# Performance work log

Measured on AMD Instinct MI355X. Metric: run time of the kernel, lower is better.

Reference implementation:

```python
import jax, jax.numpy as jnp
import numpy as np

S, L, E, H, HID, T = 4096, 16, 256, 512, 512, 50
CHAR_V = 128


def _lstm_scan(x, W_ih, W_hh, b):
    """x: [T, B, D] -> all hidden states [T, B, H]. PyTorch gate order i,f,g,o.
    b is the sum of torch's b_ih + b_hh (identical math)."""
    Hh = W_hh.shape[1]
    B = x.shape[1]

    def cell(carry, xt):
        h, c = carry
        g = xt @ W_ih.T + h @ W_hh.T + b  # [B, 4H]
        i, f, gg, o = jnp.split(g, 4, axis=-1)
        c = jax.nn.sigmoid(f) * c + jax.nn.sigmoid(i) * jnp.tanh(gg)
        h = jax.nn.sigmoid(o) * jnp.tanh(c)
        return (h, c), h

    init = (jnp.zeros((B, Hh), x.dtype), jnp.zeros((B, Hh), x.dtype))
    _, hs = jax.lax.scan(cell, init, x)
    return hs


def setup_inputs() -> dict:
    key = jax.random.key(0)
    ks = jax.random.split(key, 18)

    def p(k, shape):
        return jax.random.normal(k, shape, jnp.float32) * 0.05

    return {
        "chars": jax.random.randint(ks[0], (S, L), 0, CHAR_V),
        "char_lens": jax.random.randint(ks[1], (S,), 0, L),
        "char_table": p(ks[2], (CHAR_V, E)),
        "cW_ih": p(ks[3], (4 * E, E)),
        "cW_hh": p(ks[4], (4 * E, E)),
        "cb": p(ks[5], (4 * E,)),
        "W_ih0": p(ks[6], (2, 4 * H, E)),
        "W_hh0": p(ks[7], (2, 4 * H, H)),
        "b0": p(ks[8], (2, 4 * H)),
        "W_ih1": p(ks[9], (2, 4 * H, 2 * H)),
        "W_hh1": p(ks[10], (2, 4 * H, H)),
        "b1": p(ks[11], (2, 4 * H)),
        "fc1_w": p(ks[12], (HID, 2 * H)),
        "fc1_b": p(ks[13], (HID,)),
        "fc2_w": p(ks[14], (T, HID)),
        "fc2_b": p(ks[15], (T,)),
    }


def reference(chars, char_lens, char_table, cW_ih, cW_hh, cb,
              W_ih0, W_hh0, b0, W_ih1, W_hh1, b1,
              fc1_w, fc1_b, fc2_w, fc2_b):
    n_words = chars.shape[0]
    # --- char LSTM: batched over all words (replaces per-word python loop) ---
    emb = char_table[chars]                               # [S, L, E]
    hs = _lstm_scan(emb.transpose(1, 0, 2), cW_ih, cW_hh, cb)  # [L, S, E]
    lens = jnp.maximum(char_lens, 1)                      # every word has >=1 char
    word_emb = hs[lens - 1, jnp.arange(n_words)]          # hn per word: [S, E]

    # --- 2-layer bidirectional sentence LSTM, batch = 1 ---
    x = word_emb[:, None, :]                              # [S, 1, E]

    def bi_layer(x, Wih, Whh, b):
        fwd = _lstm_scan(x, Wih[0], Whh[0], b[0])
        bwd = _lstm_scan(x[::-1], Wih[1], Whh[1], b[1])[::-1]
        return jnp.concatenate([fwd, bwd], axis=-1)       # [S, 1, 2H]

    x = bi_layer(x, W_ih0, W_hh0, b0)
    x = bi_layer(x, W_ih1, W_hh1, b1)

    # --- MLP head ---
    out = x[:, 0, :]                                      # [S, 2H]
    out = jnp.tanh(out @ fc1_w.T + fc1_b)                 # [S, HID]
    return out @ fc2_w.T + fc2_b                          # [S, T]
```

## Files before the change

kernel.cpp:

```cpp
#include <hip/hip_runtime.h>
#include <math.h>
#include <stdint.h>


#define NPOS 4096
#define GDIM 2048

__device__ __forceinline__ float sigf(float x) { return 1.0f / (1.0f + __expf(-x)); }
__device__ __forceinline__ float tanh_fast(float x) {
  float e = __expf(2.f * x);
  return 1.f - 2.f / (e + 1.f);
}

__global__ __launch_bounds__(256) void build_wt_kernel(
    const float* __restrict__ cWih, const float* __restrict__ cWhh,
    float* __restrict__ Wt)
{
  __shared__ float tile[64][65];
  const int k0 = blockIdx.x * 64;
  const int g0 = blockIdx.y * 64;
  const float* src = (k0 < 256) ? cWih : cWhh;
  const int sk0 = k0 & 255;
  for (int i = threadIdx.x; i < 64 * 64; i += 256) {
    int r = i >> 6, cc = i & 63;
    tile[r][cc] = src[(size_t)(g0 + r) * 256 + sk0 + cc];
  }
  __syncthreads();
  for (int i = threadIdx.x; i < 64 * 64; i += 256) {
    int kk = i >> 6, gg = i & 63;
    Wt[(size_t)(k0 + kk) * 1024 + g0 + gg] = tile[gg][kk];
  }
}

__global__ __launch_bounds__(256) void char_lstm_kernel(
    const int* __restrict__ chars, const int* __restrict__ lens,
    const float* __restrict__ table, const float* __restrict__ Wt,
    const float* __restrict__ cb, float* __restrict__ word_emb)
{
  __shared__ float u[8][512];
  __shared__ float wt[8][1024];
  __shared__ int sidx[8];
  const int tid = threadIdx.x;
  const int ch = tid;
  const int w0 = blockIdx.x * 8;
  if (tid < 8) { int l = lens[w0 + tid]; sidx[tid] = (l < 1 ? 1 : l) - 1; }
  float c[8], acc0[8], acc1[8], acc2[8], acc3[8];
  #pragma unroll
  for (int w = 0; w < 8; ++w) { u[w][256 + ch] = 0.f; c[w] = 0.f; }
  const float cb0 = cb[ch], cb1 = cb[256 + ch], cb2 = cb[512 + ch], cb3 = cb[768 + ch];

  for (int t = 0; t < 16; ++t) {
    for (int w = 0; w < 8; ++w) {
      int cid = chars[(w0 + w) * 16 + t];
      u[w][ch] = table[(size_t)cid * 256 + ch];
    }
    #pragma unroll
    for (int w = 0; w < 8; ++w) { acc0[w] = cb0; acc1[w] = cb1; acc2[w] = cb2; acc3[w] = cb3; }
    for (int k0 = 0; k0 < 512; k0 += 8) {
      #pragma unroll
      for (int r = 0; r < 8; ++r)
        ((float4*)&wt[r][0])[tid] = ((const float4*)(Wt + (size_t)(k0 + r) * 1024))[tid];
      __syncthreads();
      #pragma unroll
      for (int kk = 0; kk < 8; ++kk) {
        const float wv0 = wt[kk][ch], wv1 = wt[kk][256 + ch];
        const float wv2 = wt[kk][512 + ch], wv3 = wt[kk][768 + ch];
        #pragma unroll
        for (int w = 0; w < 8; ++w) {
          const float uv = u[w][k0 + kk];
          acc0[w] = fmaf(wv0, uv, acc0[w]);
          acc1[w] = fmaf(wv1, uv, acc1[w]);
          acc2[w] = fmaf(wv2, uv, acc2[w]);
          acc3[w] = fmaf(wv3, uv, acc3[w]);
        }
      }
      __syncthreads();
    }
    #pragma unroll
    for (int w = 0; w < 8; ++w) {
      float iv = sigf(acc0[w]), fv = sigf(acc1[w]);
      float gv = tanhf(acc2[w]), ov = sigf(acc3[w]);
      c[w] = fv * c[w] + iv * gv;
      float h = ov * tanhf(c[w]);
      u[w][256 + ch] = h;
      if (t == sidx[w]) word_emb[(size_t)(w0 + w) * 256 + ch] = h;
    }
  }
}

#define SW(c) ((c) + (((c) >> 3) << 2))
template <int SPLIT, int ACT, int PERM>
__global__ __launch_bounds__(256) void gemm_kernel(
    const float* __restrict__ A, const float* __restrict__ A2,
    const float* __restrict__ B, const float* __restrict__ bias,
    float* __restrict__ C, int M, int N, int K)
{
  __shared__ float At[8 * 192];
  __shared__ float Bt[8 * 192];
  const int tid = threadIdx.x;
  const int bm0 = blockIdx.x * 128, bn0 = blockIdx.y * 128;
  float acc[8][8];
  #pragma unroll
  for (int i = 0; i < 8; ++i)
    #pragma unroll
    for (int j = 0; j < 8; ++j) acc[i][j] = 0.f;
  const int sr = tid >> 1;
  const int sk = (tid & 1) * 4;
  const int tm = (tid >> 4) * 8, tn = (tid & 15) * 8;
  const int swsr = SW(sr);
  const int stm = SW(tm), stn = SW(tn);
  for (int k0 = 0; k0 < K; k0 += 8) {
    const int kg = k0 + sk;
    float4 av;
    if (SPLIT) {
      const float* srcp = (kg < 512) ? A : A2;
      av = *(const float4*)(srcp + (size_t)(bm0 + sr) * 512 + (kg & 511));
    } else {
      av = *(const float4*)(A + (size_t)(bm0 + sr) * K + kg);
    }
    float4 bv = {0.f, 0.f, 0.f, 0.f};
    if (bn0 + sr < N) bv = *(const float4*)(B + (size_t)(bn0 + sr) * K + kg);
    At[(sk + 0) * 192 + swsr] = av.x; At[(sk + 1) * 192 + swsr] = av.y;
    At[(sk + 2) * 192 + swsr] = av.z; At[(sk + 3) * 192 + swsr] = av.w;
    Bt[(sk + 0) * 192 + swsr] = bv.x; Bt[(sk + 1) * 192 + swsr] = bv.y;
    Bt[(sk + 2) * 192 + swsr] = bv.z; Bt[(sk + 3) * 192 + swsr] = bv.w;
    __syncthreads();
    #pragma unroll
    for (int kk = 0; kk < 8; ++kk) {
      float a[8], b[8];
      *(float4*)&a[0] = *(const float4*)&At[kk * 192 + stm];
      *(float4*)&a[4] = *(const float4*)&At[kk * 192 + stm + 4];
      *(float4*)&b[0] = *(const float4*)&Bt[kk * 192 + stn];
      *(float4*)&b[4] = *(const float4*)&Bt[kk * 192 + stn + 4];
      #pragma unroll
      for (int i = 0; i < 8; ++i)
        #pragma unroll
        for (int j = 0; j < 8; ++j) acc[i][j] = fmaf(a[i], b[j], acc[i][j]);
    }
    __syncthreads();
  }
  #pragma unroll
  for (int i = 0; i < 8; ++i) {
    const int m = bm0 + tm + i;
    float* crow = C + (size_t)m * N;
    #pragma unroll
    for (int j = 0; j < 8; ++j) {
      const int n = bn0 + tn + j;
      if (n < N) {
        float v = acc[i][j] + bias[n];
        if (ACT) v = tanhf(v);
        if (PERM) crow[((n & 511) << 2) | (n >> 9)] = v;
        else      crow[n] = v;
      }
    }
  }
}

__global__ __launch_bounds__(512) void scan_kernel(
    const float* __restrict__ Xf, const float* __restrict__ Xb,
    const float* __restrict__ Whf, const float* __restrict__ Whb,
    unsigned long long* __restrict__ Tf, unsigned long long* __restrict__ Tb,
    float* __restrict__ Hf, float* __restrict__ Hb)
{
  __shared__ float lds_h[2][576];
  const int tid = threadIdx.x;
  const int dir = blockIdx.x & 1;
  const int wg  = blockIdx.x >> 1;
  const float* X = dir ? Xb : Xf;
  const float* Wh = dir ? Whb : Whf;
  unsigned long long* T = dir ? Tb : Tf;
  float* Hd = dir ? Hb : Hf;

  const int row8 = tid >> 3;
  const int klane = tid & 7;
  const int u = row8 >> 2, g = row8 & 3;
  const int R = g * 512 + wg * 16 + u;

  float wreg[64];
  {
    const float* wrow = Wh + (size_t)R * 512 + klane * 64;
    #pragma unroll
    for (int i = 0; i < 16; ++i) {
      float4 v = ((const float4*)wrow)[i];
      wreg[4 * i] = v.x; wreg[4 * i + 1] = v.y; wreg[4 * i + 2] = v.z; wreg[4 * i + 3] = v.w;
    }
  }
  const int l0 = 72 * klane;
  const int l1 = l0 + 36;
  const int la = tid + ((tid >> 5) << 2);
  const int rep = wg & 3;

  for (int i = tid; i < 576; i += 512) lds_h[0][i] = 0.f;

  const bool xl = (klane == 0);
  const int xoff = wg * 64 + row8;
  float xcur = 0.f, xnxt = 0.f;
  if (xl) {
    xcur = X[(size_t)(dir ? NPOS - 1 : 0) * GDIM + xoff];
    xnxt = X[(size_t)(dir ? NPOS - 2 : 1) * GDIM + xoff];
  }
  float creg = 0.f;
  __syncthreads();

  for (int s = 0; s < NPOS; ++s) {
    const int p = dir ? (NPOS - 1 - s) : s;
    if (s > 0) {
      const unsigned int tg = (unsigned int)s;
      const unsigned long long* w =
          T + (size_t)((rep << 1) | ((s - 1) & 1)) * 512 + tid;
      unsigned long long v;
      do { v = __hip_atomic_load(w, __ATOMIC_RELAXED, __HIP_MEMORY_SCOPE_AGENT); }
      while ((unsigned int)(v >> 32) != tg);
      lds_h[s & 1][la] = __uint_as_float((unsigned int)v);
    }
    __syncthreads();
    const float* hb = &lds_h[s & 1][0];
    float sA = xl ? xcur : 0.f, sB = 0.f, sC = 0.f, sD = 0.f;
    if (xl) {
      xcur = xnxt;
      if (s + 2 < NPOS) xnxt = X[(size_t)(dir ? NPOS - 3 - s : s + 2) * GDIM + xoff];
    }
    #pragma unroll
    for (int i = 0; i < 4; ++i) {
      float4 a = *(const float4*)&hb[l0 + 4 * i];
      sA = fmaf(wreg[4 * i + 0], a.x, sA);
      sA = fmaf(wreg[4 * i + 1], a.y, sA);
      sA = fmaf(wreg[4 * i + 2], a.z, sA);
      sA = fmaf(wreg[4 * i + 3], a.w, sA);
      float4 b = *(const float4*)&hb[l0 + 16 + 4 * i];
      sB = fmaf(wreg[16 + 4 * i + 0], b.x, sB);
      sB = fmaf(wreg[16 + 4 * i + 1], b.y, sB);
      sB = fmaf(wreg[16 + 4 * i + 2], b.z, sB);
      sB = fmaf(wreg[16 + 4 * i + 3], b.w, sB);
      float4 c = *(const float4*)&hb[l1 + 4 * i];
      sC = fmaf(wreg[32 + 4 * i + 0], c.x, sC);
      sC = fmaf(wreg[32 + 4 * i + 1], c.y, sC);
      sC = fmaf(wreg[32 + 4 * i + 2], c.z, sC);
      sC = fmaf(wreg[32 + 4 * i + 3], c.w, sC);
      float4 d = *(const float4*)&hb[l1 + 16 + 4 * i];
      sD = fmaf(wreg[48 + 4 * i + 0], d.x, sD);
      sD = fmaf(wreg[48 + 4 * i + 1], d.y, sD);
      sD = fmaf(wreg[48 + 4 * i + 2], d.z, sD);
      sD = fmaf(wreg[48 + 4 * i + 3], d.w, sD);
    }
    float sum = (sA + sB) + (sC + sD);
    sum += __shfl_xor(sum, 1);
    sum += __shfl_xor(sum, 2);
    sum += __shfl_xor(sum, 4);
    const int base = (tid & 63) & ~31;
    float gf = __shfl(sum, base + 8);
    float gg = __shfl(sum, base + 16);
    float go = __shfl(sum, base + 24);
    if ((tid & 31) == 0) {
      float iv = sigf(sum), fv = sigf(gf), gv = tanh_fast(gg), ov = sigf(go);
      creg = fv * creg + iv * gv;
      float h = ov * tanh_fast(creg);
      const int j = wg * 16 + u;
      unsigned long long pack = ((unsigned long long)(unsigned int)(s + 1) << 32)
                              | (unsigned long long)__float_as_uint(h);
      #pragma unroll
      for (int r2 = 0; r2 < 4; ++r2)
        __hip_atomic_store(&T[(size_t)((r2 << 1) | (s & 1)) * 512 + j], pack,
                           __ATOMIC_RELAXED, __HIP_MEMORY_SCOPE_AGENT);
      Hd[(size_t)p * 512 + j] = h;
    }
  }
}

extern "C" void kernel_launch(void* const* d_in, const int* in_sizes, int n_in,
                              void* d_out, int out_size, void* d_ws, size_t ws_size,
                              hipStream_t stream) {
  const int* chars = (const int*)d_in[0];
  const int* lens = (const int*)d_in[1];
  const float* table = (const float*)d_in[2];
  const float* cWih = (const float*)d_in[3];
  const float* cWhh = (const float*)d_in[4];
  const float* cb = (const float*)d_in[5];
  const float* Wih0 = (const float*)d_in[6];
  const float* Whh0 = (const float*)d_in[7];
  const float* b0 = (const float*)d_in[8];
  const float* Wih1 = (const float*)d_in[9];
  const float* Whh1 = (const float*)d_in[10];
  const float* b1 = (const float*)d_in[11];
  const float* fc1w = (const float*)d_in[12];
  const float* fc1b = (const float*)d_in[13];
  const float* fc2w = (const float*)d_in[14];
  const float* fc2b = (const float*)d_in[15];
  float* out = (float*)d_out;

  char* ws = (char*)d_ws;
  size_t off = 0;
  auto alloc = [&](size_t bytes) -> void* {
    void* p = ws + off;
    off += (bytes + 255) & ~(size_t)255;
    return p;
  };
  float* word_emb = (float*)alloc((size_t)4096 * 256 * 4);
  float* X0f = (float*)alloc((size_t)4096 * 2048 * 4);
  float* X0b = (float*)alloc((size_t)4096 * 2048 * 4);
  float* H0f = (float*)alloc((size_t)4096 * 512 * 4);
  float* H0b = (float*)alloc((size_t)4096 * 512 * 4);
  float* H1f = (float*)alloc((size_t)4096 * 512 * 4);
  float* H1b = (float*)alloc((size_t)4096 * 512 * 4);
  float* fc1out = (float*)alloc((size_t)4096 * 512 * 4);
  float* Wt = (float*)alloc((size_t)512 * 1024 * 4);
  unsigned long long* Tall = (unsigned long long*)alloc((size_t)4 * 4096 * 8);
  unsigned long long* T0f = Tall;
  unsigned long long* T0b = Tall + 4096;
  unsigned long long* T1f = Tall + 8192;
  unsigned long long* T1b = Tall + 12288;
  if (off > ws_size) return;

  hipMemsetAsync(Tall, 0, (size_t)4 * 4096 * 8, stream);

  build_wt_kernel<<<dim3(8, 16), 256, 0, stream>>>(cWih, cWhh, Wt);
  char_lstm_kernel<<<512, 256, 0, stream>>>(chars, lens, table, Wt, cb, word_emb);

  gemm_kernel<0, 0, 1><<<dim3(32, 16), 256, 0, stream>>>(
      word_emb, nullptr, Wih0, b0, X0f, 4096, 2048, 256);
  gemm_kernel<0, 0, 1><<<dim3(32, 16), 256, 0, stream>>>(
      word_emb, nullptr, Wih0 + (size_t)2048 * 256, b0 + 2048, X0b, 4096, 2048, 256);
  scan_kernel<<<64, 512, 0, stream>>>(X0f, X0b, Whh0, Whh0 + (size_t)2048 * 512,
                                      T0f, T0b, H0f, H0b);

  gemm_kernel<1, 0, 1><<<dim3(32, 16), 256, 0, stream>>>(
      H0f, H0b, Wih1, b1, X0f, 4096, 2048, 1024);
  gemm_kernel<1, 0, 1><<<dim3(32, 16), 256, 0, stream>>>(
      H0f, H0b, Wih1 + (size_t)2048 * 1024, b1 + 2048, X0b, 4096, 2048, 1024);
  scan_kernel<<<64, 512, 0, stream>>>(X0f, X0b, Whh1, Whh1 + (size_t)2048 * 512,
                                      T1f, T1b, H1f, H1b);

  gemm_kernel<1, 1, 0><<<dim3(32, 4), 256, 0, stream>>>(
      H1f, H1b, fc1w, fc1b, fc1out, 4096, 512, 1024);
  gemm_kernel<0, 0, 0><<<dim3(32, 1), 256, 0, stream>>>(
      fc1out, nullptr, fc2w, fc2b, out, 4096, 50, 512);
}
```

Before: 16.06 ms.

## Co-locate each scan direction on one XCD and use per-step L2-local flags

The scan grid is enlarged so that, with blockIdx & 7 selecting a slot, only slots 0 and 1 do work; this appears intended to place all forward blocks on one XCD and all backward blocks on another, so they can exchange hidden states through that XCD's shared L2 instead of device-scope atomics. The exchange buffer becomes one slot per timestep, tagged with the position, which removes the 4-way replicated stores and the double-buffer reuse. Polling uses inline-asm loads with sc0 and falls back to agent-scope atomic loads after 512 spins. In exchange, the flag buffer grows to 64 MB and must be memset every call, and correctness relies on the block-to-XCD placement and cache bits behaving as assumed.

```diff
diff --git a/kernel.cpp b/kernel.cpp
--- a/kernel.cpp
+++ b/kernel.cpp
@@ -162,10 +162,12 @@
     unsigned long long* __restrict__ Tf, unsigned long long* __restrict__ Tb,
     float* __restrict__ Hf, float* __restrict__ Hb)
 {
+  const int slot = blockIdx.x & 7;
+  if (slot >= 2) return;
+  const int dir = slot;
+  const int wg  = blockIdx.x >> 3;
   __shared__ float lds_h[2][576];
   const int tid = threadIdx.x;
-  const int dir = blockIdx.x & 1;
-  const int wg  = blockIdx.x >> 1;
   const float* X = dir ? Xb : Xf;
   const float* Wh = dir ? Whb : Whf;
   unsigned long long* T = dir ? Tb : Tf;
@@ -188,7 +190,6 @@
   const int l0 = 72 * klane;
   const int l1 = l0 + 36;
   const int la = tid + ((tid >> 5) << 2);
-  const int rep = wg & 3;
 
   for (int i = tid; i < 576; i += 512) lds_h[0][i] = 0.f;
 
@@ -200,17 +201,29 @@
     xnxt = X[(size_t)(dir ? NPOS - 2 : 1) * GDIM + xoff];
   }
   float creg = 0.f;
+  bool loc_ok = true;
   __syncthreads();
 
   for (int s = 0; s < NPOS; ++s) {
     const int p = dir ? (NPOS - 1 - s) : s;
     if (s > 0) {
-      const unsigned int tg = (unsigned int)s;
-      const unsigned long long* w =
-          T + (size_t)((rep << 1) | ((s - 1) & 1)) * 512 + tid;
+      const int pprev = dir ? (NPOS - s) : (s - 1);
+      const unsigned int tg = (unsigned int)(pprev + 1);
+      const unsigned long long* wp = T + (size_t)pprev * 512 + tid;
       unsigned long long v;
-      do { v = __hip_atomic_load(w, __ATOMIC_RELAXED, __HIP_MEMORY_SCOPE_AGENT); }
-      while ((unsigned int)(v >> 32) != tg);
+      if (loc_ok) {
+        int spins = 0;
+        for (;;) {
+          asm volatile("global_load_dwordx2 %0, %1, off sc0\n\ts_waitcnt vmcnt(0)"
+                       : "=v"(v) : "v"(wp) : "memory");
+          if ((unsigned int)(v >> 32) == tg) break;
+          if (++spins > 512) { loc_ok = false; break; }
+        }
+      }
+      if (!loc_ok) {
+        do { v = __hip_atomic_load(wp, __ATOMIC_RELAXED, __HIP_MEMORY_SCOPE_AGENT); }
+        while ((unsigned int)(v >> 32) != tg);
+      }
       lds_h[s & 1][la] = __uint_as_float((unsigned int)v);
     }
     __syncthreads();
@@ -256,12 +269,11 @@
       creg = fv * creg + iv * gv;
       float h = ov * tanh_fast(creg);
       const int j = wg * 16 + u;
-      unsigned long long pack = ((unsigned long long)(unsigned int)(s + 1) << 32)
+      unsigned long long pack = ((unsigned long long)(unsigned int)(p + 1) << 32)
                               | (unsigned long long)__float_as_uint(h);
-      #pragma unroll
-      for (int r2 = 0; r2 < 4; ++r2)
-        __hip_atomic_store(&T[(size_t)((r2 << 1) | (s & 1)) * 512 + j], pack,
-                           __ATOMIC_RELAXED, __HIP_MEMORY_SCOPE_AGENT);
+      unsigned long long* sp = T + (size_t)p * 512 + j;
+      asm volatile("global_store_dwordx2 %0, %1, off sc0" :: "v"(sp), "v"(pack) : "memory");
+      asm volatile("global_store_dwordx2 %0, %1, off sc0 sc1" :: "v"(sp), "v"(pack) : "memory");
       Hd[(size_t)p * 512 + j] = h;
     }
   }
@@ -304,14 +316,14 @@
   float* H1b = (float*)alloc((size_t)4096 * 512 * 4);
   float* fc1out = (float*)alloc((size_t)4096 * 512 * 4);
   float* Wt = (float*)alloc((size_t)512 * 1024 * 4);
-  unsigned long long* Tall = (unsigned long long*)alloc((size_t)4 * 4096 * 8);
+  unsigned long long* Tall = (unsigned long long*)alloc((size_t)4 * 4096 * 512 * 8);
   unsigned long long* T0f = Tall;
-  unsigned long long* T0b = Tall + 4096;
-  unsigned long long* T1f = Tall + 8192;
-  unsigned long long* T1b = Tall + 12288;
+  unsigned long long* T0b = Tall + (size_t)4096 * 512;
+  unsigned long long* T1f = Tall + (size_t)2 * 4096 * 512;
+  unsigned long long* T1b = Tall + (size_t)3 * 4096 * 512;
   if (off > ws_size) return;
 
-  hipMemsetAsync(Tall, 0, (size_t)4 * 4096 * 8, stream);
+  hipMemsetAsync(Tall, 0, (size_t)4 * 4096 * 512 * 8, stream);
 
   build_wt_kernel<<<dim3(8, 16), 256, 0, stream>>>(cWih, cWhh, Wt);
   char_lstm_kernel<<<512, 256, 0, stream>>>(chars, lens, table, Wt, cb, word_emb);
@@ -320,15 +332,15 @@
       word_emb, nullptr, Wih0, b0, X0f, 4096, 2048, 256);
   gemm_kernel<0, 0, 1><<<dim3(32, 16), 256, 0, stream>>>(
       word_emb, nullptr, Wih0 + (size_t)2048 * 256, b0 + 2048, X0b, 4096, 2048, 256);
-  scan_kernel<<<64, 512, 0, stream>>>(X0f, X0b, Whh0, Whh0 + (size_t)2048 * 512,
-                                      T0f, T0b, H0f, H0b);
+  scan_kernel<<<256, 512, 0, stream>>>(X0f, X0b, Whh0, Whh0 + (size_t)2048 * 512,
+                                       T0f, T0b, H0f, H0b);
 
   gemm_kernel<1, 0, 1><<<dim3(32, 16), 256, 0, stream>>>(
       H0f, H0b, Wih1, b1, X0f, 4096, 2048, 1024);
   gemm_kernel<1, 0, 1><<<dim3(32, 16), 256, 0, stream>>>(
       H0f, H0b, Wih1 + (size_t)2048 * 1024, b1 + 2048, X0b, 4096, 2048, 1024);
-  scan_kernel<<<64, 512, 0, stream>>>(X0f, X0b, Whh1, Whh1 + (size_t)2048 * 512,
-                                      T1f, T1b, H1f, H1b);
+  scan_kernel<<<256, 512, 0, stream>>>(X0f, X0b, Whh1, Whh1 + (size_t)2048 * 512,
+                                       T1f, T1b, H1f, H1b);
 
   gemm_kernel<1, 1, 0><<<dim3(32, 4), 256, 0, stream>>>(
       H1f, H1b, fc1w, fc1b, fc1out, 4096, 512, 1024);
```

After: 36.99 ms. 2.3x slower.

## Replace FP32 SIMT input-projection GEMMs with bf16 MFMA GEMM kernel

Applied to the files above, without the earlier changes.

Adds a new GEMM kernel that converts fp32 A and B tiles to bf16 in LDS and computes 128x128 output tiles with 16x16x32 bf16 MFMA instructions. It replaces the scalar-FMA GEMM for the four LSTM input projections and the fc1 layer. The aim is to cut the non-recurrent GEMM time by using matrix cores. In exchange, inputs are rounded to bf16, which lowers precision, and the kernel has no double buffering, so global-load latency is not overlapped.

```diff
diff --git a/kernel.cpp b/kernel.cpp
--- a/kernel.cpp
+++ b/kernel.cpp
@@ -5,11 +5,20 @@
 
 #define NPOS 4096
 #define GDIM 2048
+
+typedef short short8 __attribute__((ext_vector_type(8)));
+typedef float f32x4 __attribute__((ext_vector_type(4)));
 
 __device__ __forceinline__ float sigf(float x) { return 1.0f / (1.0f + __expf(-x)); }
 __device__ __forceinline__ float tanh_fast(float x) {
   float e = __expf(2.f * x);
   return 1.f - 2.f / (e + 1.f);
+}
+__device__ __forceinline__ unsigned int pack_bf16(float a, float b) {
+  unsigned int ua = __float_as_uint(a), ub = __float_as_uint(b);
+  ua = (ua + 0x7fffu + ((ua >> 16) & 1u)) >> 16;
+  ub = (ub + 0x7fffu + ((ub >> 16) & 1u)) >> 16;
+  return ua | (ub << 16);
 }
 
 __global__ __launch_bounds__(256) void build_wt_kernel(
@@ -151,6 +160,99 @@
         if (ACT) v = tanhf(v);
         if (PERM) crow[((n & 511) << 2) | (n >> 9)] = v;
         else      crow[n] = v;
+      }
+    }
+  }
+}
+
+template <int SPLIT, int ACT, int PERM>
+__global__ __launch_bounds__(256) void mfgemm_kernel(
+    const float* __restrict__ A, const float* __restrict__ A2,
+    const float* __restrict__ B, const float* __restrict__ bias,
+    float* __restrict__ C, int M, int N, int K)
+{
+  __shared__ unsigned short AL[128 * 40];
+  __shared__ unsigned short BL[128 * 40];
+  const int tid = threadIdx.x;
+  const int bm0 = blockIdx.x * 128, bn0 = blockIdx.y * 128;
+  const int srow = tid >> 1;
+  const int sk = (tid & 1) * 16;
+  const int lane = tid & 63;
+  const int wid = tid >> 6;
+  const int wm0 = (wid >> 1) * 64;
+  const int wn0 = (wid & 1) * 64;
+  const int lrow = lane & 15;
+  const int lk = (lane >> 4) * 8;
+
+  f32x4 acc[4][4];
+  #pragma unroll
+  for (int i = 0; i < 4; ++i)
+    #pragma unroll
+    for (int j = 0; j < 4; ++j) acc[i][j] = (f32x4){0.f, 0.f, 0.f, 0.f};
+
+  for (int k0 = 0; k0 < K; k0 += 32) {
+    const int kg = k0 + sk;
+    float av[16], bv[16];
+    if (SPLIT) {
+      const float* srcp = (kg < 512) ? A : A2;
+      const float* ap = srcp + (size_t)(bm0 + srow) * 512 + (kg & 511);
+      #pragma unroll
+      for (int i = 0; i < 4; ++i) *(float4*)&av[4 * i] = ((const float4*)ap)[i];
+      const float* srcq = (kg < 512) ? B : (B + 512);
+      (void)srcq;
+    } else {
+      const float* ap = A + (size_t)(bm0 + srow) * K + kg;
+      #pragma unroll
+      for (int i = 0; i < 4; ++i) *(float4*)&av[4 * i] = ((const float4*)ap)[i];
+    }
+    {
+      const float* bp = B + (size_t)(bn0 + srow) * K + kg;
+      #pragma unroll
+      for (int i = 0; i < 4; ++i) *(float4*)&bv[4 * i] = ((const float4*)bp)[i];
+    }
+    unsigned int pa[8], pb[8];
+    #pragma unroll
+    for (int i = 0; i < 8; ++i) {
+      pa[i] = pack_bf16(av[2 * i], av[2 * i + 1]);
+      pb[i] = pack_bf16(bv[2 * i], bv[2 * i + 1]);
+    }
+    unsigned short* adst = &AL[srow * 40 + sk];
+    unsigned short* bdst = &BL[srow * 40 + sk];
+    *(uint4*)adst       = *(uint4*)&pa[0];
+    *(uint4*)(adst + 8) = *(uint4*)&pa[4];
+    *(uint4*)bdst       = *(uint4*)&pb[0];
+    *(uint4*)(bdst + 8) = *(uint4*)&pb[4];
+    __syncthreads();
+
+    short8 af[4], bf[4];
+    #pragma unroll
+    for (int mi = 0; mi < 4; ++mi)
+      af[mi] = *(const short8*)&AL[(wm0 + mi * 16 + lrow) * 40 + lk];
+    #pragma unroll
+    for (int ni = 0; ni < 4; ++ni)
+      bf[ni] = *(const short8*)&BL[(wn0 + ni * 16 + lrow) * 40 + lk];
+    #pragma unroll
+    for (int mi = 0; mi < 4; ++mi)
+      #pragma unroll
+      for (int ni = 0; ni < 4; ++ni)
+        acc[mi][ni] = __builtin_amdgcn_mfma_f32_16x16x32_bf16(
+            af[mi], bf[ni], acc[mi][ni], 0, 0, 0);
+    __syncthreads();
+  }
+
+  #pragma unroll
+  for (int mi = 0; mi < 4; ++mi) {
+    #pragma unroll
+    for (int ni = 0; ni < 4; ++ni) {
+      const int n = bn0 + wn0 + ni * 16 + (lane & 15);
+      const float bz = bias[n];
+      const int nw = PERM ? (((n & 511) << 2) | (n >> 9)) : n;
+      #pragma unroll
+      for (int r = 0; r < 4; ++r) {
+        const int m = bm0 + wm0 + mi * 16 + (lane >> 4) * 4 + r;
+        float v = acc[mi][ni][r] + bz;
+        if (ACT) v = tanhf(v);
+        C[(size_t)m * N + nw] = v;
       }
     }
   }
@@ -316,21 +418,21 @@
   build_wt_kernel<<<dim3(8, 16), 256, 0, stream>>>(cWih, cWhh, Wt);
   char_lstm_kernel<<<512, 256, 0, stream>>>(chars, lens, table, Wt, cb, word_emb);
 
-  gemm_kernel<0, 0, 1><<<dim3(32, 16), 256, 0, stream>>>(
+  mfgemm_kernel<0, 0, 1><<<dim3(32, 16), 256, 0, stream>>>(
       word_emb, nullptr, Wih0, b0, X0f, 4096, 2048, 256);
-  gemm_kernel<0, 0, 1><<<dim3(32, 16), 256, 0, stream>>>(
+  mfgemm_kernel<0, 0, 1><<<dim3(32, 16), 256, 0, stream>>>(
       word_emb, nullptr, Wih0 + (size_t)2048 * 256, b0 + 2048, X0b, 4096, 2048, 256);
   scan_kernel<<<64, 512, 0, stream>>>(X0f, X0b, Whh0, Whh0 + (size_t)2048 * 512,
                                       T0f, T0b, H0f, H0b);
 
-  gemm_kernel<1, 0, 1><<<dim3(32, 16), 256, 0, stream>>>(
+  mfgemm_kernel<1, 0, 1><<<dim3(32, 16), 256, 0, stream>>>(
       H0f, H0b, Wih1, b1, X0f, 4096, 2048, 1024);
-  gemm_kernel<1, 0, 1><<<dim3(32, 16), 256, 0, stream>>>(
+  mfgemm_kernel<1, 0, 1><<<dim3(32, 16), 256, 0, stream>>>(
       H0f, H0b, Wih1 + (size_t)2048 * 1024, b1 + 2048, X0b, 4096, 2048, 1024);
   scan_kernel<<<64, 512, 0, stream>>>(X0f, X0b, Whh1, Whh1 + (size_t)2048 * 512,
                                       T1f, T1b, H1f, H1b);
 
-  gemm_kernel<1, 1, 0><<<dim3(32, 4), 256, 0, stream>>>(
+  mfgemm_kernel<1, 1, 0><<<dim3(32, 4), 256, 0, stream>>>(
       H1f, H1b, fc1w, fc1b, fc1out, 4096, 512, 1024);
   gemm_kernel<0, 0, 0><<<dim3(32, 1), 256, 0, stream>>>(
       fc1out, nullptr, fc2w, fc2b, out, 4096, 50, 512);
```

Measured after the change: 15.44 ms. 3.9% less time.
